# Performance work log

Hardware: AMD Instinct MI355X
Metric: run time of the kernel (lower is better)

The kernel has to match this reference:

```python
import jax, jax.numpy as jnp
import numpy as np

LN_EPS = 1e-5


def setup_inputs() -> dict:
    key = jax.random.key(0)
    ks = jax.random.split(key, 5)
    B, P, C, D = 8192, 25, 256, 5
    return {
        "features": jax.random.normal(ks[0], (B, P, C), dtype=jnp.float32),
        "weights": jax.random.normal(ks[1], (P, C, C), dtype=jnp.float32) * 0.05,
        "bias": jax.random.normal(ks[2], (P, C), dtype=jnp.float32) * 0.05,
        "ln_gamma": jnp.ones((C,), dtype=jnp.float32),
        "ln_beta": jnp.zeros((C,), dtype=jnp.float32),
        "lin_w": jax.random.normal(ks[3], (D, C), dtype=jnp.float32) * 0.05,
        "lin_b": jnp.zeros((D,), dtype=jnp.float32),
    }


def reference(features, weights, bias, ln_gamma, ln_beta, lin_w, lin_b):
    # Torch: (features.unsqueeze(-1) * weights).sum(-1) + bias
    # Broadcast [B,P,C,1]*[P,C,C] then sum over last axis reduces the SAME
    # broadcast axis, so it equals features * row-sums of weights (per point).
    w_rowsum = jnp.sum(weights, axis=-1)            # [P, C]
    point_wise = features * w_rowsum + bias          # [B, P, C]
    # LayerNorm over the channel dim
    mu = jnp.mean(point_wise, axis=-1, keepdims=True)
    var = jnp.mean(jnp.square(point_wise - mu), axis=-1, keepdims=True)
    pw_norm = (point_wise - mu) * jax.lax.rsqrt(var + LN_EPS)
    pw_norm = pw_norm * ln_gamma + ln_beta
    # residual + ReLU + final linear
    h = jax.nn.relu(features + pw_norm)              # [B, P, C]
    return jnp.einsum("bpc,dc->bpd", h, lin_w) + lin_b  # [B, P, D]
```

## Files before the change

kernel.cpp:

```cpp
#include <hip/hip_runtime.h>

#define LN_EPS 1e-5f

__global__ __launch_bounds__(256) void wrowsum_kernel(
    const float* __restrict__ w, float* __restrict__ wr, int n_rows) {
  const int lane = threadIdx.x & 63;
  const int wv   = threadIdx.x >> 6;
  const int rc   = blockIdx.x * 4 + wv;
  if (rc >= n_rows) return;
  const float4 v = reinterpret_cast<const float4*>(w)[(size_t)rc * 64 + lane];
  float s = v.x + v.y + v.z + v.w;
#pragma unroll
  for (int off = 32; off; off >>= 1) s += __shfl_xor(s, off);
  if (lane == 0) wr[rc] = s;
}

__global__ __launch_bounds__(256) void fused_main(
    const float* __restrict__ features,
    const float* __restrict__ wrow,
    const float* __restrict__ bias,
    const float* __restrict__ gamma,
    const float* __restrict__ beta,
    const float* __restrict__ lin_w,
    const float* __restrict__ lin_b,
    float* __restrict__ out,
    int n_rows, int P) {
  const int lane = threadIdx.x & 63;
  const int wv   = threadIdx.x >> 6;
  const int sub  = lane & 15;
  const int rg   = lane >> 4;
  const int r    = blockIdx.x * 16 + wv * 4 + rg;
  if (r >= n_rows) return;
  const int p = r % P;

  const float4* __restrict__ f4  = reinterpret_cast<const float4*>(features);
  const float4* __restrict__ w4  = reinterpret_cast<const float4*>(wrow);
  const float4* __restrict__ b4  = reinterpret_cast<const float4*>(bias);
  const float4* __restrict__ g4  = reinterpret_cast<const float4*>(gamma);
  const float4* __restrict__ t4  = reinterpret_cast<const float4*>(beta);
  const float4* __restrict__ l4  = reinterpret_cast<const float4*>(lin_w);

  float4 f[4], wr[4], bs[4], g[4], bt[4];
#pragma unroll
  for (int i = 0; i < 4; ++i) {
    const int c4 = i * 16 + sub;
    f[i]  = f4[(size_t)r * 64 + c4];
    wr[i] = w4[(size_t)p * 64 + c4];
    bs[i] = b4[(size_t)p * 64 + c4];
    g[i]  = g4[c4];
    bt[i] = t4[c4];
  }

  float4 pw[4];
  float s1 = 0.0f, s2 = 0.0f;
#pragma unroll
  for (int i = 0; i < 4; ++i) {
    pw[i].x = fmaf(f[i].x, wr[i].x, bs[i].x);
    pw[i].y = fmaf(f[i].y, wr[i].y, bs[i].y);
    pw[i].z = fmaf(f[i].z, wr[i].z, bs[i].z);
    pw[i].w = fmaf(f[i].w, wr[i].w, bs[i].w);
    s1 += (pw[i].x + pw[i].y) + (pw[i].z + pw[i].w);
    s2 = fmaf(pw[i].x, pw[i].x, s2);
    s2 = fmaf(pw[i].y, pw[i].y, s2);
    s2 = fmaf(pw[i].z, pw[i].z, s2);
    s2 = fmaf(pw[i].w, pw[i].w, s2);
  }
#pragma unroll
  for (int off = 8; off; off >>= 1) {
    s1 += __shfl_xor(s1, off);
    s2 += __shfl_xor(s2, off);
  }
  const float mu  = s1 * (1.0f / 256.0f);
  const float var = fmaf(-mu, mu, s2 * (1.0f / 256.0f));
  const float inv = rsqrtf(var + LN_EPS);

  float4 h[4];
#pragma unroll
  for (int i = 0; i < 4; ++i) {
    h[i].x = fmaxf(fmaf((pw[i].x - mu) * inv, g[i].x, bt[i].x) + f[i].x, 0.0f);
    h[i].y = fmaxf(fmaf((pw[i].y - mu) * inv, g[i].y, bt[i].y) + f[i].y, 0.0f);
    h[i].z = fmaxf(fmaf((pw[i].z - mu) * inv, g[i].z, bt[i].z) + f[i].z, 0.0f);
    h[i].w = fmaxf(fmaf((pw[i].w - mu) * inv, g[i].w, bt[i].w) + f[i].w, 0.0f);
  }

  float acc[5];
#pragma unroll
  for (int d = 0; d < 5; ++d) {
    float a = 0.0f;
#pragma unroll
    for (int i = 0; i < 4; ++i) {
      const float4 lw = l4[d * 64 + i * 16 + sub];
      a = fmaf(h[i].x, lw.x, a);
      a = fmaf(h[i].y, lw.y, a);
      a = fmaf(h[i].z, lw.z, a);
      a = fmaf(h[i].w, lw.w, a);
    }
    acc[d] = a;
  }
#pragma unroll
  for (int off = 8; off; off >>= 1) {
#pragma unroll
    for (int d = 0; d < 5; ++d) acc[d] += __shfl_xor(acc[d], off);
  }

  if (sub < 5) {
    float v;
    switch (sub) {
      case 0:  v = acc[0]; break;
      case 1:  v = acc[1]; break;
      case 2:  v = acc[2]; break;
      case 3:  v = acc[3]; break;
      default: v = acc[4]; break;
    }
    out[(size_t)r * 5 + sub] = v + lin_b[sub];
  }
}

extern "C" void kernel_launch(void* const* d_in, const int* in_sizes, int n_in,
                              void* d_out, int out_size, void* d_ws, size_t ws_size,
                              hipStream_t stream) {
  const float* features = (const float*)d_in[0];
  const float* weights  = (const float*)d_in[1];
  const float* bias     = (const float*)d_in[2];
  const float* gamma    = (const float*)d_in[3];
  const float* beta     = (const float*)d_in[4];
  const float* lin_w    = (const float*)d_in[5];
  const float* lin_b    = (const float*)d_in[6];
  float* out = (float*)d_out;

  const int C  = 256;
  const int PC = in_sizes[2];
  const int P  = PC / C;
  const int BP = in_sizes[0] / C;

  float* wr = (float*)d_ws;

  wrowsum_kernel<<<(PC + 3) / 4, 256, 0, stream>>>(weights, wr, PC);

  fused_main<<<(BP + 15) / 16, 256, 0, stream>>>(
      features, wr, bias, gamma, beta, lin_w, lin_b, out, BP, P);
}
```

Before: 325.5 us.

## Make fused kernel persistent per point with register-prefetched feature rows

The main kernel is relaunched on a 2D grid, chunks of 64 batch rows by P points, so each block handles a single point index. The per-point weight row-sums, bias, LayerNorm params and the linear weights are loaded once into registers and reused across 4 rows per 16-lane group. The next feature row is prefetched into registers while the current one is processed, and an occupancy hint of 2 is added to launch bounds. The aim is to amortize parameter loads and hide memory latency. The cost is higher register pressure and strided feature accesses, since consecutive iterations jump 16*P rows apart.

```diff
diff --git a/kernel.cpp b/kernel.cpp
--- a/kernel.cpp
+++ b/kernel.cpp
@@ -15,7 +15,7 @@
   if (lane == 0) wr[rc] = s;
 }
 
-__global__ __launch_bounds__(256) void fused_main(
+__global__ __launch_bounds__(256, 2) void fused_main(
     const float* __restrict__ features,
     const float* __restrict__ wrow,
     const float* __restrict__ bias,
@@ -24,95 +24,120 @@
     const float* __restrict__ lin_w,
     const float* __restrict__ lin_b,
     float* __restrict__ out,
-    int n_rows, int P) {
+    int B, int P) {
   const int lane = threadIdx.x & 63;
   const int wv   = threadIdx.x >> 6;
   const int sub  = lane & 15;
-  const int rg   = lane >> 4;
-  const int r    = blockIdx.x * 16 + wv * 4 + rg;
-  if (r >= n_rows) return;
-  const int p = r % P;
+  const int grp  = wv * 4 + (lane >> 4);
+  const int p    = blockIdx.y;
 
-  const float4* __restrict__ f4  = reinterpret_cast<const float4*>(features);
-  const float4* __restrict__ w4  = reinterpret_cast<const float4*>(wrow);
-  const float4* __restrict__ b4  = reinterpret_cast<const float4*>(bias);
-  const float4* __restrict__ g4  = reinterpret_cast<const float4*>(gamma);
-  const float4* __restrict__ t4  = reinterpret_cast<const float4*>(beta);
-  const float4* __restrict__ l4  = reinterpret_cast<const float4*>(lin_w);
+  const float4* __restrict__ f4 = reinterpret_cast<const float4*>(features);
+  const float4* __restrict__ w4 = reinterpret_cast<const float4*>(wrow);
+  const float4* __restrict__ b4 = reinterpret_cast<const float4*>(bias);
+  const float4* __restrict__ g4 = reinterpret_cast<const float4*>(gamma);
+  const float4* __restrict__ t4 = reinterpret_cast<const float4*>(beta);
+  const float4* __restrict__ l4 = reinterpret_cast<const float4*>(lin_w);
 
-  float4 f[4], wr[4], bs[4], g[4], bt[4];
+  float4 wr[4], bs[4], g[4], bt[4], lw[5][4];
 #pragma unroll
   for (int i = 0; i < 4; ++i) {
     const int c4 = i * 16 + sub;
-    f[i]  = f4[(size_t)r * 64 + c4];
     wr[i] = w4[(size_t)p * 64 + c4];
     bs[i] = b4[(size_t)p * 64 + c4];
     g[i]  = g4[c4];
     bt[i] = t4[c4];
   }
+#pragma unroll
+  for (int d = 0; d < 5; ++d)
+#pragma unroll
+    for (int i = 0; i < 4; ++i) lw[d][i] = l4[d * 64 + i * 16 + sub];
+  const float lb = (sub < 5) ? lin_b[sub] : 0.0f;
 
-  float4 pw[4];
-  float s1 = 0.0f, s2 = 0.0f;
+  int b = blockIdx.x * 64 + grp;
+  const size_t fstep = (size_t)16 * P * 64;
+  const size_t ostep = (size_t)16 * P * 5;
+  const float4* fp = f4 + ((size_t)b * P + p) * 64 + sub;
+  size_t orow = ((size_t)b * P + p) * 5;
+
+  float4 fc[4], fn[4];
+  bool ok = (b < B);
+  if (ok) {
 #pragma unroll
-  for (int i = 0; i < 4; ++i) {
-    pw[i].x = fmaf(f[i].x, wr[i].x, bs[i].x);
-    pw[i].y = fmaf(f[i].y, wr[i].y, bs[i].y);
-    pw[i].z = fmaf(f[i].z, wr[i].z, bs[i].z);
-    pw[i].w = fmaf(f[i].w, wr[i].w, bs[i].w);
-    s1 += (pw[i].x + pw[i].y) + (pw[i].z + pw[i].w);
-    s2 = fmaf(pw[i].x, pw[i].x, s2);
-    s2 = fmaf(pw[i].y, pw[i].y, s2);
-    s2 = fmaf(pw[i].z, pw[i].z, s2);
-    s2 = fmaf(pw[i].w, pw[i].w, s2);
+    for (int i = 0; i < 4; ++i) fc[i] = fp[i * 16];
   }
+  fp += fstep;
+
+  for (int it = 0; it < 4; ++it) {
+    const bool okn = (b + 16 * (it + 1) < B) && (it < 3);
+    if (okn) {
 #pragma unroll
-  for (int off = 8; off; off >>= 1) {
-    s1 += __shfl_xor(s1, off);
-    s2 += __shfl_xor(s2, off);
-  }
-  const float mu  = s1 * (1.0f / 256.0f);
-  const float var = fmaf(-mu, mu, s2 * (1.0f / 256.0f));
-  const float inv = rsqrtf(var + LN_EPS);
+      for (int i = 0; i < 4; ++i) fn[i] = fp[i * 16];
+    }
+    fp += fstep;
 
-  float4 h[4];
+    if (ok) {
+      float4 pw[4];
+      float s1 = 0.0f, s2 = 0.0f;
 #pragma unroll
-  for (int i = 0; i < 4; ++i) {
-    h[i].x = fmaxf(fmaf((pw[i].x - mu) * inv, g[i].x, bt[i].x) + f[i].x, 0.0f);
-    h[i].y = fmaxf(fmaf((pw[i].y - mu) * inv, g[i].y, bt[i].y) + f[i].y, 0.0f);
-    h[i].z = fmaxf(fmaf((pw[i].z - mu) * inv, g[i].z, bt[i].z) + f[i].z, 0.0f);
-    h[i].w = fmaxf(fmaf((pw[i].w - mu) * inv, g[i].w, bt[i].w) + f[i].w, 0.0f);
-  }
+      for (int i = 0; i < 4; ++i) {
+        pw[i].x = fmaf(fc[i].x, wr[i].x, bs[i].x);
+        pw[i].y = fmaf(fc[i].y, wr[i].y, bs[i].y);
+        pw[i].z = fmaf(fc[i].z, wr[i].z, bs[i].z);
+        pw[i].w = fmaf(fc[i].w, wr[i].w, bs[i].w);
+        s1 += (pw[i].x + pw[i].y) + (pw[i].z + pw[i].w);
+        s2 = fmaf(pw[i].x, pw[i].x, s2);
+        s2 = fmaf(pw[i].y, pw[i].y, s2);
+        s2 = fmaf(pw[i].z, pw[i].z, s2);
+        s2 = fmaf(pw[i].w, pw[i].w, s2);
+      }
+#pragma unroll
+      for (int off = 8; off; off >>= 1) {
+        s1 += __shfl_xor(s1, off);
+        s2 += __shfl_xor(s2, off);
+      }
+      const float mu  = s1 * (1.0f / 256.0f);
+      const float var = fmaf(-mu, mu, s2 * (1.0f / 256.0f));
+      const float inv = rsqrtf(var + LN_EPS);
 
-  float acc[5];
+      float acc[5] = {0.0f, 0.0f, 0.0f, 0.0f, 0.0f};
 #pragma unroll
-  for (int d = 0; d < 5; ++d) {
-    float a = 0.0f;
+      for (int i = 0; i < 4; ++i) {
+        float4 h;
+        h.x = fmaxf(fmaf((pw[i].x - mu) * inv, g[i].x, bt[i].x) + fc[i].x, 0.0f);
+        h.y = fmaxf(fmaf((pw[i].y - mu) * inv, g[i].y, bt[i].y) + fc[i].y, 0.0f);
+        h.z = fmaxf(fmaf((pw[i].z - mu) * inv, g[i].z, bt[i].z) + fc[i].z, 0.0f);
+        h.w = fmaxf(fmaf((pw[i].w - mu) * inv, g[i].w, bt[i].w) + fc[i].w, 0.0f);
 #pragma unroll
-    for (int i = 0; i < 4; ++i) {
-      const float4 lw = l4[d * 64 + i * 16 + sub];
-      a = fmaf(h[i].x, lw.x, a);
-      a = fmaf(h[i].y, lw.y, a);
-      a = fmaf(h[i].z, lw.z, a);
-      a = fmaf(h[i].w, lw.w, a);
+        for (int d = 0; d < 5; ++d) {
+          acc[d] = fmaf(h.x, lw[d][i].x, acc[d]);
+          acc[d] = fmaf(h.y, lw[d][i].y, acc[d]);
+          acc[d] = fmaf(h.z, lw[d][i].z, acc[d]);
+          acc[d] = fmaf(h.w, lw[d][i].w, acc[d]);
+        }
+      }
+#pragma unroll
+      for (int off = 8; off; off >>= 1) {
+#pragma unroll
+        for (int d = 0; d < 5; ++d) acc[d] += __shfl_xor(acc[d], off);
+      }
+
+      if (sub < 5) {
+        float v;
+        switch (sub) {
+          case 0:  v = acc[0]; break;
+          case 1:  v = acc[1]; break;
+          case 2:  v = acc[2]; break;
+          case 3:  v = acc[3]; break;
+          default: v = acc[4]; break;
+        }
+        out[orow + sub] = v + lb;
+      }
     }
-    acc[d] = a;
-  }
+
 #pragma unroll
-  for (int off = 8; off; off >>= 1) {
-#pragma unroll
-    for (int d = 0; d < 5; ++d) acc[d] += __shfl_xor(acc[d], off);
-  }
-
-  if (sub < 5) {
-    float v;
-    switch (sub) {
-      case 0:  v = acc[0]; break;
-      case 1:  v = acc[1]; break;
-      case 2:  v = acc[2]; break;
-      case 3:  v = acc[3]; break;
-      default: v = acc[4]; break;
-    }
-    out[(size_t)r * 5 + sub] = v + lin_b[sub];
+    for (int i = 0; i < 4; ++i) fc[i] = fn[i];
+    ok = okn;
+    orow += ostep;
   }
 }
 
@@ -132,11 +157,13 @@
   const int PC = in_sizes[2];
   const int P  = PC / C;
   const int BP = in_sizes[0] / C;
+  const int B  = BP / P;
 
   float* wr = (float*)d_ws;
 
   wrowsum_kernel<<<(PC + 3) / 4, 256, 0, stream>>>(weights, wr, PC);
 
-  fused_main<<<(BP + 15) / 16, 256, 0, stream>>>(
-      features, wr, bias, gamma, beta, lin_w, lin_b, out, BP, P);
+  const int chunks = (B + 63) / 64;
+  fused_main<<<dim3(chunks, P), 256, 0, stream>>>(
+      features, wr, bias, gamma, beta, lin_w, lin_b, out, B, P);
 }
```

After: 315.3 us. -3.1%, faster.
